# Kernel tuning notes

Hardware: AMD Instinct MI355X
Metric: run time of the kernel (lower is better)

Reference implementation:

```python
import jax, jax.numpy as jnp
import numpy as np
from jax import lax

B, PN, NS = 8, 16384, 256
KDIM, HID = 512, 384
HALF = HID // 2
EPS = 1e-5


def setup_inputs() -> dict:
    key = jax.random.key(0)
    ks = jax.random.split(key, 12)
    s = lambda fan: np.float32(1.0 / np.sqrt(fan))
    inp = {
        "p": jax.random.normal(ks[0], (B, PN, 3), jnp.float32),
        "N": NS,
        "patch_feature": jax.random.normal(ks[1], (B, KDIM, 1), jnp.float32),
        # Linear(k_dim, hidden)
        "W_feat": jax.random.normal(ks[2], (KDIM, HID), jnp.float32) * s(KDIM),
        "b_feat": jax.random.normal(ks[3], (HID,), jnp.float32) * s(KDIM),
        # Linear(3, hidden//2)
        "W_coord": jax.random.normal(ks[4], (3, HALF), jnp.float32) * s(3),
        "b_coord": jax.random.normal(ks[5], (HALF,), jnp.float32) * s(3),
        # Conv1d(hidden+hidden//2, hidden, 1) == per-point linear, weight (out,in)
        "W1": jax.random.normal(ks[6], (HID, HID + HALF), jnp.float32) * s(HID + HALF),
        "b1": jax.random.normal(ks[7], (HID,), jnp.float32) * s(HID + HALF),
        "g1": jnp.ones((HID,), jnp.float32),
        "be1": jnp.zeros((HID,), jnp.float32),
        # Conv1d(hidden, hidden, 1)
        "W2": jax.random.normal(ks[8], (HID, HID), jnp.float32) * s(HID),
        "b2": jax.random.normal(ks[9], (HID,), jnp.float32) * s(HID),
        "g2": jnp.ones((HID,), jnp.float32),
        "be2": jnp.zeros((HID,), jnp.float32),
    }
    return inp


def farthest_point_sample(points, k):
    """points: (B, N, C) -> (B, k, C). Deterministic start index 0 per batch."""
    b, n, c = points.shape

    def step(carry, _):
        dist, far = carry
        centroid = jnp.take_along_axis(points, far[:, None, None], axis=1)  # (B,1,C)
        d = jnp.sum((points - centroid) ** 2, axis=-1)                      # (B,N)
        dist = jnp.minimum(dist, d)
        new_far = jnp.argmax(dist, axis=-1)
        return (dist, new_far), far

    init = (jnp.full((b, n), 1e10, points.dtype), jnp.zeros((b,), jnp.int32))
    _, idx = lax.scan(step, init, None, length=k)  # idx: (k, B)
    idx = idx.T                                    # (B, k)
    return jnp.take_along_axis(points, idx[:, :, None], axis=1)  # (B,k,C)


def batchnorm(x, gamma, beta):
    """x: (B, L, C); training-mode BN over (B, L) per channel (biased var)."""
    mean = jnp.mean(x, axis=(0, 1))
    var = jnp.var(x, axis=(0, 1))
    return (x - mean) * lax.rsqrt(var + EPS) * gamma + beta


def reference(p, N, patch_feature, W_feat, b_feat, W_coord, b_coord,
              W1, b1, g1, be1, W2, b2, g2, be2):
    b, pn, _ = p.shape
    global_feat = patch_feature[..., 0] @ W_feat + b_feat          # (B, HID)
    global_feat = jnp.broadcast_to(global_feat[:, None, :], (b, N, HID))
    local_feat = p @ W_coord + b_coord                              # (B, PN, HALF)
    if N != pn:
        local_feat = farthest_point_sample(local_feat, N)           # (B, N, HALF)
    combined = jnp.concatenate([global_feat, local_feat], axis=-1)  # (B, N, HID+HALF)
    h = jnp.einsum("bnc,oc->bno", combined, W1) + b1
    h = jax.nn.relu(batchnorm(h, g1, be1))
    h = jnp.einsum("bnc,oc->bno", h, W2) + b2
    h = jax.nn.relu(batchnorm(h, g2, be2))
    return h  # (B, N, HID)
```

## Files before the change

### kernel.cpp

```cpp
#include <hip/hip_runtime.h>

#define BATCH 8
#define PN    16384
#define NSAMP 256
#define KDIM  512
#define HID   384
#define HALF  192
#define CIN   576
#define ROWS  2048
#define BN_EPS 1e-5f

#define OFF_GF   0
#define OFF_W1T  3072
#define OFF_GFW  76800
#define OFF_W2T  224256
#define OFF_IDX  371712
#define OFF_H1   373760
#define OFF_H2   1160192
#define OFF_SUM1 1946624
#define OFF_SQ1  1947008
#define OFF_SUM2 1947392
#define OFF_SQ2  1947776

typedef float v2f __attribute__((ext_vector_type(2)));

__global__ __launch_bounds__(512, 2) void k_main(const float* p, const float* Wc,
                                                 const float* pf, const float* Wf,
                                                 const float* bfe, const float* W1,
                                                 const float* b1v, const float* W2,
                                                 float* ws) {
  __shared__ float s[KDIM];
  __shared__ float Msh[6];
  __shared__ __align__(16) float redv[2][8];
  __shared__ int widx[2];
  int blk = blockIdx.x, t = threadIdx.x;

  if (blk >= 8) {
    if (blk < 16) {
      for (int sI = (blk - 8) * 512 + t; sI < HID * HALF; sI += 4096) {
        int o = sI / HALF, c = sI % HALF;
        ws[OFF_W1T + c * HID + o] = W1[o * CIN + HID + c];
      }
    } else if (blk < 24) {
      for (int sI = (blk - 16) * 512 + t; sI < HID * HID; sI += 4096) {
        int o = sI / HID, c = sI % HID;
        ws[OFF_W2T + c * HID + o] = W2[sI];
      }
    } else if (blk < 32) {
      int b = blk - 24;
      if (t < KDIM) s[t] = pf[b * KDIM + t];
      __syncthreads();
      float acc = 0.f;
      if (t < HID) {
        acc = bfe[t];
        for (int k = 0; k < KDIM; k++) acc = fmaf(s[k], Wf[k * HID + t], acc);
        ws[OFF_GF + b * HID + t] = acc;
      }
      __syncthreads();
      if (t < HID) s[t] = acc;
      __syncthreads();
      if (t < HID) {
        float g = b1v[t];
        const float* w1row = W1 + t * CIN;
        for (int c = 0; c < HID; c++) g = fmaf(s[c], w1row[c], g);
        ws[OFF_GFW + b * HID + t] = g;
      }
    } else {
      for (int i = t; i < 1536; i += 512) ws[OFF_SUM1 + i] = 0.f;
    }
    return;
  }

  int b = blk;
  int* idx_out = (int*)(ws + OFF_IDX);

  if (t < 64) {
    double g0 = 0, g1 = 0, g2 = 0, g3 = 0, g4 = 0, g5 = 0;
    for (int k = t; k < HALF; k += 64) {
      double w0 = (double)Wc[k];
      double w1 = (double)Wc[HALF + k];
      double w2 = (double)Wc[2 * HALF + k];
      g0 += w0 * w0; g1 += w0 * w1; g2 += w0 * w2;
      g3 += w1 * w1; g4 += w1 * w2; g5 += w2 * w2;
    }
    for (int off = 32; off; off >>= 1) {
      g0 += __shfl_down(g0, off, 64); g1 += __shfl_down(g1, off, 64);
      g2 += __shfl_down(g2, off, 64); g3 += __shfl_down(g3, off, 64);
      g4 += __shfl_down(g4, off, 64); g5 += __shfl_down(g5, off, 64);
    }
    if (t == 0) {
      double l00 = sqrt(g0);
      double l10 = g1 / l00, l20 = g2 / l00;
      double l11 = sqrt(g3 - l10 * l10);
      double l21 = (g4 - l10 * l20) / l11;
      double l22 = sqrt(g5 - l20 * l20 - l21 * l21);
      Msh[0] = (float)l00; Msh[1] = (float)l10; Msh[2] = (float)l20;
      Msh[3] = (float)l11; Msh[4] = (float)l21; Msh[5] = (float)l22;
    }
  }
  __syncthreads();
  float m00 = Msh[0], m10 = Msh[1], m20 = Msh[2];
  float m11 = Msh[3], m21 = Msh[4], m22 = Msh[5];

  const float* pb = p + b * PN * 3;
  float4* qws = (float4*)(ws + OFF_H1) + b * PN;
  v2f qx[16], qy[16], qz[16], nq[16], dist[16];
#pragma unroll
  for (int j = 0; j < 16; j++) {
    int i0 = (j << 10) + t;
    int i1 = i0 + 512;
    float x0 = pb[i0 * 3], y0 = pb[i0 * 3 + 1], z0 = pb[i0 * 3 + 2];
    float x1 = pb[i1 * 3], y1 = pb[i1 * 3 + 1], z1 = pb[i1 * 3 + 2];
    qx[j] = (v2f){fmaf(m00, x0, fmaf(m10, y0, m20 * z0)),
                  fmaf(m00, x1, fmaf(m10, y1, m20 * z1))};
    qy[j] = (v2f){fmaf(m11, y0, m21 * z0), fmaf(m11, y1, m21 * z1)};
    qz[j] = (v2f){m22 * z0, m22 * z1};
    nq[j] = __builtin_elementwise_fma(
        qx[j], qx[j],
        __builtin_elementwise_fma(qy[j], qy[j], qz[j] * qz[j]));
    dist[j] = (v2f){1e10f, 1e10f};
    qws[i0] = make_float4(qx[j].x, qy[j].x, qz[j].x, nq[j].x);
    qws[i1] = make_float4(qx[j].y, qy[j].y, qz[j].y, nq[j].y);
  }

  if (t == 0) { widx[1] = 0; widx[0] = 0x7fffffff; }
  __syncthreads();

  int par = 0;
  for (int k = 0; k < NSAMP; k++) {
    int far = widx[par ^ 1];
    if (t == 0) {
      idx_out[b * NSAMP + k] = far;
      widx[par] = 0x7fffffff;
    }
    float4 qc = qws[far];
    float cx2 = -2.f * qc.x, cy2 = -2.f * qc.y, cz2 = -2.f * qc.z;
    v2f cxv = (v2f){cx2, cx2}, cyv = (v2f){cy2, cy2}, czv = (v2f){cz2, cz2};
    v2f ncv = (v2f){qc.w, qc.w};
#pragma unroll
    for (int j = 0; j < 16; j++) {
      v2f base = nq[j] + ncv;
      v2f d = __builtin_elementwise_fma(
          qx[j], cxv,
          __builtin_elementwise_fma(qy[j], cyv,
              __builtin_elementwise_fma(qz[j], czv, base)));
      dist[j] = __builtin_elementwise_min(dist[j], d);
    }
    v2f t0v = __builtin_elementwise_max(dist[0], dist[1]);
    v2f t1v = __builtin_elementwise_max(dist[2], dist[3]);
    v2f t2v = __builtin_elementwise_max(dist[4], dist[5]);
    v2f t3v = __builtin_elementwise_max(dist[6], dist[7]);
    v2f t4v = __builtin_elementwise_max(dist[8], dist[9]);
    v2f t5v = __builtin_elementwise_max(dist[10], dist[11]);
    v2f t6v = __builtin_elementwise_max(dist[12], dist[13]);
    v2f t7v = __builtin_elementwise_max(dist[14], dist[15]);
    t0v = __builtin_elementwise_max(t0v, t1v);
    t2v = __builtin_elementwise_max(t2v, t3v);
    t4v = __builtin_elementwise_max(t4v, t5v);
    t6v = __builtin_elementwise_max(t6v, t7v);
    t0v = __builtin_elementwise_max(t0v, t2v);
    t4v = __builtin_elementwise_max(t4v, t6v);
    t0v = __builtin_elementwise_max(t0v, t4v);
    float tmax = fmaxf(t0v.x, t0v.y);
    float m = tmax;
#pragma unroll
    for (int off = 32; off; off >>= 1) m = fmaxf(m, __shfl_xor(m, off, 64));
    if ((t & 63) == 0) redv[par][t >> 6] = m;
    __syncthreads();
    float4 r0 = *(const float4*)&redv[par][0];
    float4 r1 = *(const float4*)&redv[par][4];
    float g01 = fmaxf(fmaxf(r0.x, r0.y), fmaxf(r0.z, r0.w));
    float g02 = fmaxf(fmaxf(r1.x, r1.y), fmaxf(r1.z, r1.w));
    float gmax = fmaxf(g01, g02);
    if (tmax == gmax) {
      int mi = 0x7fffffff;
#pragma unroll
      for (int j = 15; j >= 0; j--) {
        int i0 = (j << 10) + t;
        mi = (dist[j].y == gmax) ? i0 + 512 : mi;
        mi = (dist[j].x == gmax) ? i0 : mi;
      }
      atomicMin(&widx[par], mi);
    }
    __syncthreads();
    par ^= 1;
  }
}

__global__ __launch_bounds__(384) void k_gemm1(const float* p,
                                               const float* Wc,
                                               const float* bc,
                                               float* ws) {
  __shared__ __align__(16) float ct[HALF * 8];
  int t = threadIdx.x;
  int row0 = blockIdx.x * 8;
  int b = row0 >> 8;
  const int* fidx = (const int*)(ws + OFF_IDX);
  for (int sI = t; sI < 8 * HALF; sI += 384) {
    int r = sI / HALF, co = sI % HALF;
    int row = row0 + r;
    int i = fidx[row];
    const float* pp = p + (b * PN + i) * 3;
    float val = bc[co];
    val = fmaf(pp[0], Wc[co], val);
    val = fmaf(pp[1], Wc[HALF + co], val);
    val = fmaf(pp[2], Wc[2 * HALF + co], val);
    ct[co * 8 + r] = val;
  }
  __syncthreads();
  const float* w1t = ws + OFF_W1T;
  float acc[8] = {0.f, 0.f, 0.f, 0.f, 0.f, 0.f, 0.f, 0.f};
  for (int c = 0; c < HALF; c++) {
    float w = w1t[c * HID + t];
    float4 a0 = *(const float4*)(ct + c * 8);
    float4 a1 = *(const float4*)(ct + c * 8 + 4);
    acc[0] = fmaf(a0.x, w, acc[0]); acc[1] = fmaf(a0.y, w, acc[1]);
    acc[2] = fmaf(a0.z, w, acc[2]); acc[3] = fmaf(a0.w, w, acc[3]);
    acc[4] = fmaf(a1.x, w, acc[4]); acc[5] = fmaf(a1.y, w, acc[5]);
    acc[6] = fmaf(a1.z, w, acc[6]); acc[7] = fmaf(a1.w, w, acc[7]);
  }
  float base = ws[OFF_GFW + b * HID + t];
  float sv = 0.f, sq = 0.f;
#pragma unroll
  for (int r = 0; r < 8; r++) {
    float v = acc[r] + base;
    ws[OFF_H1 + (row0 + r) * HID + t] = v;
    sv += v; sq = fmaf(v, v, sq);
  }
  atomicAdd(&ws[OFF_SUM1 + t], sv);
  atomicAdd(&ws[OFF_SQ1 + t], sq);
}

__global__ __launch_bounds__(384) void k_gemm2(const float* b2,
                                               const float* g1,
                                               const float* be1,
                                               float* ws) {
  __shared__ __align__(16) float ht[HID * 8];
  __shared__ float sc1s[HID], sh1s[HID];
  int t = threadIdx.x;
  int row0 = blockIdx.x * 8;
  {
    float m = ws[OFF_SUM1 + t] * (1.f / ROWS);
    float v = ws[OFF_SQ1 + t] * (1.f / ROWS) - m * m;
    float inv = 1.f / sqrtf(v + BN_EPS);
    float sc = inv * g1[t];
    sc1s[t] = sc;
    sh1s[t] = be1[t] - m * sc;
  }
  __syncthreads();
  for (int sI = t; sI < 8 * HID; sI += 384) {
    int r = sI / HID, c = sI % HID;
    float x = fmaf(ws[OFF_H1 + (row0 + r) * HID + c], sc1s[c], sh1s[c]);
    ht[c * 8 + r] = fmaxf(x, 0.f);
  }
  __syncthreads();
  const float* w2t = ws + OFF_W2T;
  float acc[8] = {0.f, 0.f, 0.f, 0.f, 0.f, 0.f, 0.f, 0.f};
  for (int c = 0; c < HID; c++) {
    float w = w2t[c * HID + t];
    float4 a0 = *(const float4*)(ht + c * 8);
    float4 a1 = *(const float4*)(ht + c * 8 + 4);
    acc[0] = fmaf(a0.x, w, acc[0]); acc[1] = fmaf(a0.y, w, acc[1]);
    acc[2] = fmaf(a0.z, w, acc[2]); acc[3] = fmaf(a0.w, w, acc[3]);
    acc[4] = fmaf(a1.x, w, acc[4]); acc[5] = fmaf(a1.y, w, acc[5]);
    acc[6] = fmaf(a1.z, w, acc[6]); acc[7] = fmaf(a1.w, w, acc[7]);
  }
  float bias = b2[t];
  float sv = 0.f, sq = 0.f;
#pragma unroll
  for (int r = 0; r < 8; r++) {
    float v = acc[r] + bias;
    ws[OFF_H2 + (row0 + r) * HID + t] = v;
    sv += v; sq = fmaf(v, v, sq);
  }
  atomicAdd(&ws[OFF_SUM2 + t], sv);
  atomicAdd(&ws[OFF_SQ2 + t], sq);
}

__global__ __launch_bounds__(256) void k_out(const float* ws, const float* g2,
                                             const float* be2, float* out) {
  int gid = blockIdx.x * 256 + threadIdx.x;
  int i = gid * 4;
  int c = i % HID;
  float4 h  = *(const float4*)(ws + OFF_H2 + i);
  float4 s2 = *(const float4*)(ws + OFF_SUM2 + c);
  float4 q2 = *(const float4*)(ws + OFF_SQ2 + c);
  float4 gv = *(const float4*)(g2 + c);
  float4 bv = *(const float4*)(be2 + c);
  float4 r;
#define BN2(comp) {                                                  \
    float m  = s2.comp * (1.f / ROWS);                               \
    float v  = q2.comp * (1.f / ROWS) - m * m;                       \
    float sc = (1.f / sqrtf(v + BN_EPS)) * gv.comp;                  \
    float sh = bv.comp - m * sc;                                     \
    r.comp = fmaxf(fmaf(h.comp, sc, sh), 0.f); }
  BN2(x) BN2(y) BN2(z) BN2(w)
#undef BN2
  ((float4*)out)[gid] = r;
}

extern "C" void kernel_launch(void* const* d_in, const int* in_sizes, int n_in,
                              void* d_out, int out_size, void* d_ws, size_t ws_size,
                              hipStream_t stream) {
  const float* p   = (const float*)d_in[0];
  const float* pf  = (const float*)d_in[2];
  const float* Wf  = (const float*)d_in[3];
  const float* bfe = (const float*)d_in[4];
  const float* Wc  = (const float*)d_in[5];
  const float* bc  = (const float*)d_in[6];
  const float* W1  = (const float*)d_in[7];
  const float* b1  = (const float*)d_in[8];
  const float* g1  = (const float*)d_in[9];
  const float* be1 = (const float*)d_in[10];
  const float* W2  = (const float*)d_in[11];
  const float* b2  = (const float*)d_in[12];
  const float* g2  = (const float*)d_in[13];
  const float* be2 = (const float*)d_in[14];
  float* ws = (float*)d_ws;

  hipLaunchKernelGGL(k_main,  dim3(33),  dim3(512), 0, stream,
                     p, Wc, pf, Wf, bfe, W1, b1, W2, ws);
  hipLaunchKernelGGL(k_gemm1, dim3(256), dim3(384), 0, stream, p, Wc, bc, ws);
  hipLaunchKernelGGL(k_gemm2, dim3(256), dim3(384), 0, stream, b2, g1, be1, ws);
  hipLaunchKernelGGL(k_out,   dim3(768), dim3(256), 0, stream,
                     ws, g2, be2, (float*)d_out);
}
```

Baseline: 526.3 us.

## Widen FPS block to 1024 threads and use DPP wave reduction

The farthest-point-sampling block now runs with 1024 threads, so each thread keeps 16 points in registers instead of 32. This halves the per-thread serial distance update in each of the 256 dependent iterations. The intra-wave max reduction switches from shuffles to DPP row operations, and the load of the selected centroid is hoisted above the thread-0 bookkeeping. In exchange, the cross-wave reduction now reads 16 wave maxima, and the block barrier covers twice as many waves.

```diff
diff --git a/kernel.cpp b/kernel.cpp
--- a/kernel.cpp
+++ b/kernel.cpp
@@ -24,25 +24,29 @@
 
 typedef float v2f __attribute__((ext_vector_type(2)));
 
-__global__ __launch_bounds__(512, 2) void k_main(const float* p, const float* Wc,
-                                                 const float* pf, const float* Wf,
-                                                 const float* bfe, const float* W1,
-                                                 const float* b1v, const float* W2,
-                                                 float* ws) {
+#define DPP_MAX(v, ctrl)                                                   \
+  v = fmaxf(v, __int_as_float(__builtin_amdgcn_update_dpp(                 \
+          0, __float_as_int(v), (ctrl), 0xf, 0xf, true)))
+
+__global__ __launch_bounds__(1024, 4) void k_main(const float* p, const float* Wc,
+                                                  const float* pf, const float* Wf,
+                                                  const float* bfe, const float* W1,
+                                                  const float* b1v, const float* W2,
+                                                  float* ws) {
   __shared__ float s[KDIM];
   __shared__ float Msh[6];
-  __shared__ __align__(16) float redv[2][8];
+  __shared__ __align__(16) float redv[2][16];
   __shared__ int widx[2];
   int blk = blockIdx.x, t = threadIdx.x;
 
   if (blk >= 8) {
     if (blk < 16) {
-      for (int sI = (blk - 8) * 512 + t; sI < HID * HALF; sI += 4096) {
+      for (int sI = (blk - 8) * 1024 + t; sI < HID * HALF; sI += 8192) {
         int o = sI / HALF, c = sI % HALF;
         ws[OFF_W1T + c * HID + o] = W1[o * CIN + HID + c];
       }
     } else if (blk < 24) {
-      for (int sI = (blk - 16) * 512 + t; sI < HID * HID; sI += 4096) {
+      for (int sI = (blk - 16) * 1024 + t; sI < HID * HID; sI += 8192) {
         int o = sI / HID, c = sI % HID;
         ws[OFF_W2T + c * HID + o] = W2[sI];
       }
@@ -66,7 +70,7 @@
         ws[OFF_GFW + b * HID + t] = g;
       }
     } else {
-      for (int i = t; i < 1536; i += 512) ws[OFF_SUM1 + i] = 0.f;
+      for (int i = t; i < 1536; i += 1024) ws[OFF_SUM1 + i] = 0.f;
     }
     return;
   }
@@ -104,11 +108,11 @@
 
   const float* pb = p + b * PN * 3;
   float4* qws = (float4*)(ws + OFF_H1) + b * PN;
-  v2f qx[16], qy[16], qz[16], nq[16], dist[16];
-#pragma unroll
-  for (int j = 0; j < 16; j++) {
-    int i0 = (j << 10) + t;
-    int i1 = i0 + 512;
+  v2f qx[8], qy[8], qz[8], nq[8], dist[8];
+#pragma unroll
+  for (int j = 0; j < 8; j++) {
+    int i0 = ((2 * j) << 10) + t;
+    int i1 = i0 + 1024;
     float x0 = pb[i0 * 3], y0 = pb[i0 * 3 + 1], z0 = pb[i0 * 3 + 2];
     float x1 = pb[i1 * 3], y1 = pb[i1 * 3 + 1], z1 = pb[i1 * 3 + 2];
     qx[j] = (v2f){fmaf(m00, x0, fmaf(m10, y0, m20 * z0)),
@@ -129,16 +133,16 @@
   int par = 0;
   for (int k = 0; k < NSAMP; k++) {
     int far = widx[par ^ 1];
+    float4 qc = qws[far];
     if (t == 0) {
       idx_out[b * NSAMP + k] = far;
       widx[par] = 0x7fffffff;
     }
-    float4 qc = qws[far];
     float cx2 = -2.f * qc.x, cy2 = -2.f * qc.y, cz2 = -2.f * qc.z;
     v2f cxv = (v2f){cx2, cx2}, cyv = (v2f){cy2, cy2}, czv = (v2f){cz2, cz2};
     v2f ncv = (v2f){qc.w, qc.w};
 #pragma unroll
-    for (int j = 0; j < 16; j++) {
+    for (int j = 0; j < 8; j++) {
       v2f base = nq[j] + ncv;
       v2f d = __builtin_elementwise_fma(
           qx[j], cxv,
@@ -150,34 +154,34 @@
     v2f t1v = __builtin_elementwise_max(dist[2], dist[3]);
     v2f t2v = __builtin_elementwise_max(dist[4], dist[5]);
     v2f t3v = __builtin_elementwise_max(dist[6], dist[7]);
-    v2f t4v = __builtin_elementwise_max(dist[8], dist[9]);
-    v2f t5v = __builtin_elementwise_max(dist[10], dist[11]);
-    v2f t6v = __builtin_elementwise_max(dist[12], dist[13]);
-    v2f t7v = __builtin_elementwise_max(dist[14], dist[15]);
     t0v = __builtin_elementwise_max(t0v, t1v);
     t2v = __builtin_elementwise_max(t2v, t3v);
-    t4v = __builtin_elementwise_max(t4v, t5v);
-    t6v = __builtin_elementwise_max(t6v, t7v);
     t0v = __builtin_elementwise_max(t0v, t2v);
-    t4v = __builtin_elementwise_max(t4v, t6v);
-    t0v = __builtin_elementwise_max(t0v, t4v);
     float tmax = fmaxf(t0v.x, t0v.y);
-    float m = tmax;
-#pragma unroll
-    for (int off = 32; off; off >>= 1) m = fmaxf(m, __shfl_xor(m, off, 64));
-    if ((t & 63) == 0) redv[par][t >> 6] = m;
+    float wv = tmax;
+    DPP_MAX(wv, 0x111);
+    DPP_MAX(wv, 0x112);
+    DPP_MAX(wv, 0x114);
+    DPP_MAX(wv, 0x118);
+    DPP_MAX(wv, 0x142);
+    DPP_MAX(wv, 0x143);
+    if ((t & 63) == 63) redv[par][t >> 6] = wv;
     __syncthreads();
     float4 r0 = *(const float4*)&redv[par][0];
     float4 r1 = *(const float4*)&redv[par][4];
+    float4 r2 = *(const float4*)&redv[par][8];
+    float4 r3 = *(const float4*)&redv[par][12];
     float g01 = fmaxf(fmaxf(r0.x, r0.y), fmaxf(r0.z, r0.w));
     float g02 = fmaxf(fmaxf(r1.x, r1.y), fmaxf(r1.z, r1.w));
-    float gmax = fmaxf(g01, g02);
+    float g03 = fmaxf(fmaxf(r2.x, r2.y), fmaxf(r2.z, r2.w));
+    float g04 = fmaxf(fmaxf(r3.x, r3.y), fmaxf(r3.z, r3.w));
+    float gmax = fmaxf(fmaxf(g01, g02), fmaxf(g03, g04));
     if (tmax == gmax) {
       int mi = 0x7fffffff;
 #pragma unroll
-      for (int j = 15; j >= 0; j--) {
-        int i0 = (j << 10) + t;
-        mi = (dist[j].y == gmax) ? i0 + 512 : mi;
+      for (int j = 7; j >= 0; j--) {
+        int i0 = ((2 * j) << 10) + t;
+        mi = (dist[j].y == gmax) ? i0 + 1024 : mi;
         mi = (dist[j].x == gmax) ? i0 : mi;
       }
       atomicMin(&widx[par], mi);
@@ -318,7 +322,7 @@
   const float* be2 = (const float*)d_in[14];
   float* ws = (float*)d_ws;
 
-  hipLaunchKernelGGL(k_main,  dim3(33),  dim3(512), 0, stream,
+  hipLaunchKernelGGL(k_main,  dim3(33),  dim3(1024), 0, stream,
                      p, Wc, pf, Wf, bfe, W1, b1, W2, ws);
   hipLaunchKernelGGL(k_gemm1, dim3(256), dim3(384), 0, stream, p, Wc, bc, ws);
   hipLaunchKernelGGL(k_gemm2, dim3(256), dim3(384), 0, stream, b2, g1, be1, ws);
```

New measurement: 514.3 us. 1.02x faster.
